# Optimization experiments

Measured on AMD Instinct MI355X. Metric: run time of the kernel, lower is better.

Reference implementation:

```python
import jax, jax.numpy as jnp
import numpy as np

B, M, D = 8, 1024, 1024
H = 16
HD = D // H  # 64
F = 4096

def layer_norm(x, gamma, beta, eps=1e-5):
    mu = jnp.mean(x, axis=-1, keepdims=True)
    var = jnp.var(x, axis=-1, keepdims=True)
    return (x - mu) * jax.lax.rsqrt(var + eps) * gamma + beta

def setup_inputs() -> dict:
    key = jax.random.key(0)
    ks = jax.random.split(key, 16)
    s = 0.02
    return {
        "h": jax.random.normal(ks[0], (B, M, D), jnp.float32),
        "h_all": jax.random.normal(ks[1], (B, M, D), jnp.float32),
        "Wq": jax.random.normal(ks[2], (D, D), jnp.float32) * s,
        "Wk": jax.random.normal(ks[3], (D, D), jnp.float32) * s,
        "Wv": jax.random.normal(ks[4], (D, D), jnp.float32) * s,
        "Wo": jax.random.normal(ks[5], (D, D), jnp.float32) * s,
        "W1": jax.random.normal(ks[6], (D, F), jnp.float32) * s,
        "b1": jnp.zeros((F,), jnp.float32),
        "W2": jax.random.normal(ks[7], (F, D), jnp.float32) * s,
        "b2": jnp.zeros((D,), jnp.float32),
        "g1": jnp.ones((D,), jnp.float32),
        "be1": jnp.zeros((D,), jnp.float32),
        "g2": jnp.ones((D,), jnp.float32),
        "be2": jnp.zeros((D,), jnp.float32),
    }

def reference(h, h_all, Wq, Wk, Wv, Wo, W1, b1, W2, b2, g1, be1, g2, be2):
    Bx, Mx, Dx = h.shape
    # projections (no bias, per nn.Linear(bias=False))
    q = (h @ Wq).reshape(Bx, Mx, H, HD)        # [B,M,H,hd]
    k = (h_all @ Wk).reshape(Bx, -1, H, HD)    # [B,N,H,hd]
    v = (h_all @ Wv).reshape(Bx, -1, H, HD)
    # attention: scale by sqrt(head_dim) as in SeqAttention(hidden_size=head_dim)
    scores = jnp.einsum('bqhd,bkhd->bhqk', q, k) / jnp.sqrt(jnp.float32(HD))
    attn = jax.nn.softmax(scores, axis=-1)
    ctx = jnp.einsum('bhqk,bkhd->bqhd', attn, v).reshape(Bx, Mx, Dx)
    attn_out = ctx @ Wo
    # post-norm residual 1
    h1 = layer_norm(h + attn_out, g1, be1)
    # FFN
    ff = jax.nn.relu(h1 @ W1 + b1) @ W2 + b2
    # post-norm residual 2
    out = layer_norm(h1 + ff, g2, be2)
    return out
```

## Files before the change

### kernel.cpp

```cpp
#include <hip/hip_runtime.h>
#include <hip/hip_bf16.h>

#define ROWS 8192
#define DD   1024
#define HH   16
#define HD   64
#define FF   4096

typedef __attribute__((ext_vector_type(4))) float f32x4;
typedef __attribute__((ext_vector_type(8))) __bf16 bf16x8;

static __device__ __forceinline__ unsigned short f2bf(float f) {
  unsigned u = __float_as_uint(f);
  u += 0x7fffu + ((u >> 16) & 1u);
  return (unsigned short)(u >> 16);
}

static __device__ __forceinline__ float bf2f(unsigned short u) {
  return __uint_as_float(((unsigned)u) << 16);
}

static __device__ __forceinline__ unsigned cvtpk_bf16(float lo, float hi) {
  unsigned r;
  asm("v_cvt_pk_bf16_f32 %0, %1, %2" : "=v"(r) : "v"(lo), "v"(hi));
  return r;
}

static __device__ __forceinline__ f32x4 mfma16(bf16x8 a, bf16x8 b, f32x4 c) {
  return __builtin_amdgcn_mfma_f32_16x16x32_bf16(a, b, c, 0, 0, 0);
}

#define GLOAD16(gp, lp) __builtin_amdgcn_global_load_lds( \
    (__attribute__((address_space(1))) void*)(gp), \
    (__attribute__((address_space(3))) void*)(lp), 16, 0, 0)

__global__ __launch_bounds__(256) void prep_k(
    const float* __restrict__ h, const float* __restrict__ hall,
    const float* __restrict__ Wq, const float* __restrict__ Wk,
    const float* __restrict__ Wv, const float* __restrict__ Wo,
    const float* __restrict__ W1, const float* __restrict__ W2,
    unsigned short* __restrict__ hb, unsigned short* __restrict__ hab,
    unsigned short* __restrict__ wqt, unsigned short* __restrict__ wkvt,
    unsigned short* __restrict__ wot, unsigned short* __restrict__ w1t,
    unsigned short* __restrict__ w2t) {
  __shared__ unsigned short tile[64][66];
  const int bid = blockIdx.x;
  const int tid = threadIdx.x;

  if (bid < 16384) {
    const float* src = (bid < 8192) ? h : hall;
    unsigned short* dst = (bid < 8192) ? hb : hab;
    int i = (bid & 8191) * 256 + tid;
    float4 v = ((const float4*)src)[i];
    ushort4 o;
    o.x = f2bf(v.x); o.y = f2bf(v.y); o.z = f2bf(v.z); o.w = f2bf(v.w);
    ((ushort4*)dst)[i] = o;
    return;
  }

  int r = bid - 16384;
  const float* src; unsigned short* dst; int R, C, bx, by;
  if (r < 1024) {
    int which = r >> 8, idx = r & 255;
    R = C = 1024; bx = idx & 15; by = idx >> 4;
    if (which == 0) { src = Wq; dst = wqt; }
    else if (which == 1) { src = Wk; dst = wkvt; }
    else if (which == 2) { src = Wv; dst = wkvt + (size_t)DD * DD; }
    else { src = Wo; dst = wot; }
  } else if (r < 2048) {
    int idx = r - 1024;
    R = 1024; C = 4096; bx = idx & 63; by = idx >> 6;
    src = W1; dst = w1t;
  } else {
    int idx = r - 2048;
    R = 4096; C = 1024; bx = idx & 15; by = idx >> 4;
    src = W2; dst = w2t;
  }
  const int col = tid & 63, q4 = tid >> 6;
  #pragma unroll
  for (int i = 0; i < 16; ++i) {
    int rr = q4 + i * 4;
    tile[rr][col] = f2bf(src[(size_t)(by * 64 + rr) * C + bx * 64 + col]);
  }
  __syncthreads();
  #pragma unroll
  for (int i = 0; i < 16; ++i) {
    int c = q4 + i * 4;
    dst[(size_t)(bx * 64 + c) * R + by * 64 + col] = tile[col][c];
  }
}

template <int BM, int MODE, int KS = 1>
static __device__ __forceinline__ void gemm_body(
    char* ldsA, char* ldsB,
    const unsigned short* __restrict__ A, const unsigned short* __restrict__ BT,
    const float* __restrict__ bias, void* __restrict__ Cout, void* __restrict__ Cout2,
    int Ni, int Ki, int nbx, int wg, int nwg) {
  constexpr int MR = BM / 32;

  const int tid  = threadIdx.x;
  const int lane = tid & 63;
  const int wid  = tid >> 6;
  const int wm   = wid >> 2;
  const int wn   = wid & 3;
  const int lr   = lane & 15;
  const int kq   = lane >> 4;
  const int axor = (lr & 7) << 4;

  const int cpx = nwg >> 3;
  const int swz = (wg & 7) * cpx + (wg >> 3);
  const int perk = nwg / KS;
  const int kh   = swz / perk;
  const int swzr = swz % perk;
  const int bx = swzr % nbx, by = swzr / nbx;
  const int brow = by * BM, bcol = bx * 256;
  const int Kc   = Ki / KS;
  const int kbase = kh * Kc;

  f32x4 acc[MR][4] = {};
  const int NT = Kc >> 6;

  if constexpr (BM == 256) {
    const size_t loff = (size_t)(lane >> 3) * Ki + ((lane & 7) ^ (lane >> 3)) * 8;
    const unsigned short* Ab = A + (size_t)brow * Ki + kbase;
    const unsigned short* Bb = BT + (size_t)bcol * Ki + kbase;

    auto stage2 = [&](int qc, int u, int db) {
      const int ra = ((wid & 4) << 5) + qc * 32 + (wid & 3) * 8;
      GLOAD16(Ab + (size_t)ra * Ki + u * 64 + loff, ldsA + db * 32768 + ra * 128);
      const int rb = qc * 64 + wid * 8;
      GLOAD16(Bb + (size_t)rb * Ki + u * 64 + loff, ldsB + db * 32768 + rb * 128);
    };

    #pragma unroll
    for (int qc = 0; qc < 4; ++qc) stage2(qc, 0, 0);
    {
      const int u1 = (1 < NT) ? 1 : NT - 1;
      stage2(0, u1, 1); stage2(1, u1, 1); stage2(2, u1, 1);
    }
    asm volatile("s_waitcnt vmcnt(6)" ::: "memory");
    __builtin_amdgcn_s_barrier();
    __builtin_amdgcn_sched_barrier(0);

    #pragma unroll 1
    for (int t = 0; t < NT; ++t) {
      const int d = t & 1;
      const char* ab = ldsA + d * 32768;
      const char* bb = ldsB + d * 32768;
      bf16x8 bfv[4][2];
      #pragma unroll
      for (int q = 0; q < 4; ++q) {
        bf16x8 af[2][2];
        #pragma unroll
        for (int mm = 0; mm < 2; ++mm)
          #pragma unroll
          for (int ks = 0; ks < 2; ++ks)
            af[mm][ks] = *(const bf16x8*)(ab +
                (wm * 128 + (q * 2 + mm) * 16 + lr) * 128 +
                ((ks * 64 + kq * 16) ^ axor));
        if (q == 0) {
          #pragma unroll
          for (int n = 0; n < 4; ++n)
            #pragma unroll
            for (int ks = 0; ks < 2; ++ks)
              bfv[n][ks] = *(const bf16x8*)(bb +
                  (wn * 64 + n * 16 + lr) * 128 +
                  ((ks * 64 + kq * 16) ^ axor));
        }
        if (q == 0) {
          stage2(3, (t + 1 < NT) ? t + 1 : NT - 1, (t + 1) & 1);
        } else {
          stage2(q - 1, (t + 2 < NT) ? t + 2 : NT - 1, d);
        }
        __builtin_amdgcn_s_setprio(1);
        #pragma unroll
        for (int mm = 0; mm < 2; ++mm)
          #pragma unroll
          for (int n = 0; n < 4; ++n) {
            acc[q * 2 + mm][n] = mfma16(af[mm][0], bfv[n][0], acc[q * 2 + mm][n]);
            acc[q * 2 + mm][n] = mfma16(af[mm][1], bfv[n][1], acc[q * 2 + mm][n]);
          }
        __builtin_amdgcn_s_setprio(0);
        __builtin_amdgcn_sched_barrier(0);
        if (q == 3) asm volatile("s_waitcnt vmcnt(6)" ::: "memory");
        __builtin_amdgcn_s_barrier();
        __builtin_amdgcn_sched_barrier(0);
      }
    }
    asm volatile("s_waitcnt vmcnt(0)" ::: "memory");
  } else {
    const int srow = wid * 8 + (lane >> 3);
    const int scol = ((lane & 7) * 8) ^ ((srow & 7) << 3);
    size_t offA[BM / 64], offB[4];
    #pragma unroll
    for (int L = 0; L < BM / 64; ++L)
      offA[L] = (size_t)(brow + L * 64 + srow) * Ki + kbase + scol;
    #pragma unroll
    for (int L = 0; L < 4; ++L)
      offB[L] = (size_t)(bcol + L * 64 + srow) * Ki + kbase + scol;

    auto stage = [&](int t, int d) {
      #pragma unroll
      for (int L = 0; L < BM / 64; ++L)
        GLOAD16(A + offA[L] + t * 64, ldsA + d * (BM * 128) + L * 8192 + wid * 1024);
      #pragma unroll
      for (int L = 0; L < 4; ++L)
        GLOAD16(BT + offB[L] + t * 64, ldsB + d * 32768 + L * 8192 + wid * 1024);
    };

    stage(0, 0);
    stage(1, 1);

    #pragma unroll 1
    for (int t = 0; t < NT; ++t) {
      const int d = t & 1;
      asm volatile("s_waitcnt vmcnt(6)" ::: "memory");
      __builtin_amdgcn_s_barrier();
      __builtin_amdgcn_sched_barrier(0);

      const char* as = ldsA + d * (BM * 128);
      const char* bs = ldsB + d * 32768;
      #pragma unroll
      for (int kk = 0; kk < 2; ++kk) {
        bf16x8 af[MR], bfv[4];
        #pragma unroll
        for (int m = 0; m < MR; ++m)
          af[m] = *(const bf16x8*)(as +
              (wm * (BM / 2) + m * 16 + lr) * 128 + ((kk * 64 + kq * 16) ^ axor));
        #pragma unroll
        for (int n = 0; n < 4; ++n)
          bfv[n] = *(const bf16x8*)(bs +
              (wn * 64 + n * 16 + lr) * 128 + ((kk * 64 + kq * 16) ^ axor));
        #pragma unroll
        for (int m = 0; m < MR; ++m)
          #pragma unroll
          for (int n = 0; n < 4; ++n)
            acc[m][n] = mfma16(af[m], bfv[n], acc[m][n]);
      }

      asm volatile("s_waitcnt lgkmcnt(0)" ::: "memory");
      __builtin_amdgcn_s_barrier();
      __builtin_amdgcn_sched_barrier(0);
      const int ts = (t + 2 < NT) ? t + 2 : NT - 1;
      stage(ts, d);
    }
  }

  #pragma unroll
  for (int m = 0; m < MR; ++m) {
    #pragma unroll
    for (int n = 0; n < 4; ++n) {
      const int r0 = brow + wm * (BM / 2) + m * 16 + kq * 4;
      const int c  = bcol + wn * 64 + n * 16 + lr;
      if constexpr (MODE == 4) {
        if (c < 1024) {
          #pragma unroll
          for (int e = 0; e < 4; ++e)
            ((unsigned short*)Cout)[(size_t)(r0 + e) * 1024 + c] = f2bf(acc[m][n][e]);
        } else {
          const int cc = c - 1024;
          const int bq = r0 >> 10;
          const int tok = r0 & 1023;
          ushort4 pk;
          pk.x = f2bf(acc[m][n][0]); pk.y = f2bf(acc[m][n][1]);
          pk.z = f2bf(acc[m][n][2]); pk.w = f2bf(acc[m][n][3]);
          *(ushort4*)((unsigned short*)Cout2 + ((size_t)bq * 1024 + cc) * 1024 + tok) = pk;
        }
      } else if constexpr (MODE == 5) {
        unsigned short* o = (kh == 0) ? (unsigned short*)Cout : (unsigned short*)Cout2;
        #pragma unroll
        for (int e = 0; e < 4; ++e)
          o[(size_t)(r0 + e) * Ni + c] = f2bf(acc[m][n][e]);
      } else {
        const float bv = (MODE == 2 || MODE == 3) ? bias[c] : 0.0f;
        #pragma unroll
        for (int e = 0; e < 4; ++e) {
          float v = acc[m][n][e] + bv;
          if (MODE == 2) v = fmaxf(v, 0.0f);
          if (MODE == 0 || MODE == 2)
            ((unsigned short*)Cout)[(size_t)(r0 + e) * Ni + c] = f2bf(v);
          else
            ((float*)Cout)[(size_t)(r0 + e) * Ni + c] = v;
        }
      }
    }
  }
}

template <int BM, int MODE, int KS = 1>
__global__ __launch_bounds__(512, 2) void gemm256(
    const unsigned short* __restrict__ A, const unsigned short* __restrict__ BT,
    const float* __restrict__ bias, void* __restrict__ Cout, void* __restrict__ Cout2,
    int Ni, int Ki, int nbx) {
  constexpr int ABYTES = 2 * BM * 64 * 2;
  __shared__ char lds[ABYTES + 65536];
  gemm_body<BM, MODE, KS>(lds, lds + ABYTES, A, BT, bias, Cout, Cout2,
                          Ni, Ki, nbx, (int)blockIdx.x, (int)gridDim.x);
}

__global__ __launch_bounds__(512, 2) void qkv_k(
    const unsigned short* __restrict__ hb, const unsigned short* __restrict__ hab,
    const unsigned short* __restrict__ wqt, const unsigned short* __restrict__ wkvt,
    unsigned short* __restrict__ qb, unsigned short* __restrict__ kb,
    unsigned short* __restrict__ vTb) {
  __shared__ char lds[131072];
  if (blockIdx.x < 256)
    gemm_body<256, 4, 1>(lds, lds + 65536, hab, wkvt, nullptr, kb, vTb,
                         2048, 1024, 8, (int)blockIdx.x, 256);
  else
    gemm_body<128, 0, 1>(lds, lds + 32768, hb, wqt, nullptr, qb, nullptr,
                         1024, 1024, 4, (int)blockIdx.x - 256, 256);
}

__global__ __launch_bounds__(512, 6) void attn_k(
    const unsigned short* __restrict__ q, const unsigned short* __restrict__ k,
    const unsigned short* __restrict__ vT, unsigned short* __restrict__ ctx) {
  __shared__ unsigned short Ks[2][64 * 64];
  __shared__ unsigned short Vt[2][64 * 64];
  __shared__ unsigned short Ps[8][16 * 64];
  const int tid = threadIdx.x;
  const int lane = tid & 63;
  const int wid = tid >> 6;
  const int bh = blockIdx.x;
  const int b = bh >> 4, h = bh & 15;
  const int qrow0 = blockIdx.y * 128 + wid * 16;
  const size_t tokbase = (size_t)b * 1024;
  const int lr = lane & 15, kq = lane >> 4;

  const int srow = tid >> 3;
  const int scol = ((tid & 7) * 8) ^ ((srow & 7) << 3);
  const unsigned short* kg = k + (tokbase + srow) * 1024 + h * 64 + scol;
  const unsigned short* vg = vT + ((size_t)(b * 16 + h) * 64 + srow) * 1024 + scol;
  const int ldst = tid * 16;

  auto stage = [&](int kt, int d) {
    GLOAD16(kg + (size_t)kt * 64 * 1024, (char*)Ks[d] + ldst);
    GLOAD16(vg + kt * 64, (char*)Vt[d] + ldst);
  };

  bf16x8 aq[2];
  {
    const unsigned short* qp = q + (tokbase + qrow0 + lr) * DD + h * 64 + kq * 8;
    aq[0] = *(const bf16x8*)qp;
    aq[1] = *(const bf16x8*)(qp + 32);
  }

  float l_acc = 0.f;
  f32x4 acc[4] = {};
  const float C = 0.125f * 1.4426950408889634f;
  const unsigned swp = (unsigned)((lr & 7) << 4);
  const unsigned pbase = (unsigned)(lr * 128);

  stage(0, 0);
  stage(1, 1);

  #pragma unroll 2
  for (int kt = 0; kt < 16; ++kt) {
    const int d = kt & 1;
    asm volatile("s_waitcnt vmcnt(2)" ::: "memory");
    __builtin_amdgcn_s_barrier();
    __builtin_amdgcn_sched_barrier(0);

    f32x4 sv[4] = {};
    __builtin_amdgcn_s_setprio(1);
    #pragma unroll
    for (int jb = 0; jb < 4; ++jb)
      #pragma unroll
      for (int ks = 0; ks < 2; ++ks) {
        int row = jb * 16 + lr;
        bf16x8 ak = *(const bf16x8*)((const char*)Ks[d] +
            row * 128 + ((ks * 64 + kq * 16) ^ ((row & 7) << 4)));
        sv[jb] = mfma16(ak, aq[ks], sv[jb]);
      }
    __builtin_amdgcn_s_setprio(0);

    #pragma unroll
    for (int jb = 0; jb < 4; ++jb) {
      float p0 = exp2f(sv[jb][0] * C);
      float p1 = exp2f(sv[jb][1] * C);
      float p2 = exp2f(sv[jb][2] * C);
      float p3 = exp2f(sv[jb][3] * C);
      l_acc += (p0 + p1) + (p2 + p3);
      uint2 w;
      w.x = cvtpk_bf16(p0, p1);
      w.y = cvtpk_bf16(p2, p3);
      unsigned off = pbase + (((unsigned)(jb * 32 + kq * 8)) ^ swp);
      *(uint2*)((char*)Ps[wid] + off) = w;
    }

    __builtin_amdgcn_s_setprio(1);
    #pragma unroll
    for (int ks = 0; ks < 2; ++ks) {
      bf16x8 ap = *(const bf16x8*)((const char*)Ps[wid] +
          lr * 128 + ((ks * 64 + kq * 16) ^ ((lr & 7) << 4)));
      #pragma unroll
      for (int db = 0; db < 4; ++db) {
        int dd = db * 16 + lr;
        bf16x8 bv = *(const bf16x8*)((const char*)Vt[d] +
            dd * 128 + ((ks * 64 + kq * 16) ^ ((dd & 7) << 4)));
        acc[db] = mfma16(bv, ap, acc[db]);
      }
    }
    __builtin_amdgcn_s_setprio(0);

    asm volatile("s_waitcnt lgkmcnt(0)" ::: "memory");
    __builtin_amdgcn_s_barrier();
    __builtin_amdgcn_sched_barrier(0);
    const int ts = (kt + 2 < 16) ? kt + 2 : 15;
    stage(ts, d);
  }

  float l = l_acc + __shfl_xor(l_acc, 16);
  l += __shfl_xor(l, 32);
  const float inv = 1.0f / l;
  unsigned short* cp = ctx + (tokbase + qrow0 + lr) * DD + h * 64 + kq * 4;
  #pragma unroll
  for (int db = 0; db < 4; ++db) {
    ushort4 o;
    o.x = f2bf(acc[db][0] * inv);
    o.y = f2bf(acc[db][1] * inv);
    o.z = f2bf(acc[db][2] * inv);
    o.w = f2bf(acc[db][3] * inv);
    *(ushort4*)(cp + db * 16) = o;
  }
}

__global__ __launch_bounds__(256) void ln_add_bb_k(
    const unsigned short* __restrict__ a, const unsigned short* __restrict__ b,
    const float* __restrict__ gamma, const float* __restrict__ beta,
    unsigned short* __restrict__ outb) {
  int row = blockIdx.x;
  int tid = threadIdx.x;
  size_t base = (size_t)row * 1024 + tid * 4;
  ushort4 va = *(const ushort4*)(a + base);
  ushort4 vb = *(const ushort4*)(b + base);
  float x[4] = {bf2f(va.x) + bf2f(vb.x), bf2f(va.y) + bf2f(vb.y),
                bf2f(va.z) + bf2f(vb.z), bf2f(va.w) + bf2f(vb.w)};
  float s = x[0] + x[1] + x[2] + x[3];
  float sq = x[0] * x[0] + x[1] * x[1] + x[2] * x[2] + x[3] * x[3];
  #pragma unroll
  for (int mk = 1; mk < 64; mk <<= 1) {
    s += __shfl_xor(s, mk);
    sq += __shfl_xor(sq, mk);
  }
  __shared__ float red[8];
  int wid = tid >> 6, lane = tid & 63;
  if (lane == 0) { red[wid] = s; red[4 + wid] = sq; }
  __syncthreads();
  s = red[0] + red[1] + red[2] + red[3];
  sq = red[4] + red[5] + red[6] + red[7];
  float mu = s * (1.0f / 1024.0f);
  float var = sq * (1.0f / 1024.0f) - mu * mu;
  float rs = rsqrtf(var + 1e-5f);
  float4 g = *(const float4*)(gamma + tid * 4);
  float4 be = *(const float4*)(beta + tid * 4);
  ushort4 ob;
  ob.x = f2bf((x[0] - mu) * rs * g.x + be.x);
  ob.y = f2bf((x[1] - mu) * rs * g.y + be.y);
  ob.z = f2bf((x[2] - mu) * rs * g.z + be.z);
  ob.w = f2bf((x[3] - mu) * rs * g.w + be.w);
  *(ushort4*)(outb + base) = ob;
}

__global__ __launch_bounds__(256) void ln3_k(
    const unsigned short* __restrict__ a, const unsigned short* __restrict__ p0,
    const unsigned short* __restrict__ p1, const float* __restrict__ b2,
    const float* __restrict__ gamma, const float* __restrict__ beta,
    float* __restrict__ outf) {
  int row = blockIdx.x;
  int tid = threadIdx.x;
  size_t base = (size_t)row * 1024 + tid * 4;
  ushort4 va = *(const ushort4*)(a + base);
  ushort4 v0 = *(const ushort4*)(p0 + base);
  ushort4 v1 = *(const ushort4*)(p1 + base);
  float4 bb = *(const float4*)(b2 + tid * 4);
  float x[4] = {bf2f(va.x) + bf2f(v0.x) + bf2f(v1.x) + bb.x,
                bf2f(va.y) + bf2f(v0.y) + bf2f(v1.y) + bb.y,
                bf2f(va.z) + bf2f(v0.z) + bf2f(v1.z) + bb.z,
                bf2f(va.w) + bf2f(v0.w) + bf2f(v1.w) + bb.w};
  float s = x[0] + x[1] + x[2] + x[3];
  float sq = x[0] * x[0] + x[1] * x[1] + x[2] * x[2] + x[3] * x[3];
  #pragma unroll
  for (int mk = 1; mk < 64; mk <<= 1) {
    s += __shfl_xor(s, mk);
    sq += __shfl_xor(sq, mk);
  }
  __shared__ float red[8];
  int wid = tid >> 6, lane = tid & 63;
  if (lane == 0) { red[wid] = s; red[4 + wid] = sq; }
  __syncthreads();
  s = red[0] + red[1] + red[2] + red[3];
  sq = red[4] + red[5] + red[6] + red[7];
  float mu = s * (1.0f / 1024.0f);
  float var = sq * (1.0f / 1024.0f) - mu * mu;
  float rs = rsqrtf(var + 1e-5f);
  float4 g = *(const float4*)(gamma + tid * 4);
  float4 be = *(const float4*)(beta + tid * 4);
  float4 o;
  o.x = (x[0] - mu) * rs * g.x + be.x;
  o.y = (x[1] - mu) * rs * g.y + be.y;
  o.z = (x[2] - mu) * rs * g.z + be.z;
  o.w = (x[3] - mu) * rs * g.w + be.w;
  *(float4*)(outf + base) = o;
}

extern "C" void kernel_launch(void* const* d_in, const int* in_sizes, int n_in,
                              void* d_out, int out_size, void* d_ws, size_t ws_size,
                              hipStream_t stream) {
  const float* h    = (const float*)d_in[0];
  const float* hall = (const float*)d_in[1];
  const float* Wq   = (const float*)d_in[2];
  const float* Wk   = (const float*)d_in[3];
  const float* Wv   = (const float*)d_in[4];
  const float* Wo   = (const float*)d_in[5];
  const float* W1   = (const float*)d_in[6];
  const float* b1   = (const float*)d_in[7];
  const float* W2   = (const float*)d_in[8];
  const float* b2   = (const float*)d_in[9];
  const float* g1   = (const float*)d_in[10];
  const float* be1  = (const float*)d_in[11];
  const float* g2   = (const float*)d_in[12];
  const float* be2  = (const float*)d_in[13];

  char* ws = (char*)d_ws;
  size_t off = 0;
  auto alloc = [&](size_t n) { size_t o = off; off += (n + 255) & ~(size_t)255; return o; };
  const size_t hb_o   = alloc((size_t)ROWS * DD * 2);
  const size_t hab_o  = alloc((size_t)ROWS * DD * 2);
  const size_t wqt_o  = alloc((size_t)DD * DD * 2);
  const size_t wkvt_o = alloc((size_t)DD * DD * 4);
  const size_t wot_o  = alloc((size_t)DD * DD * 2);
  const size_t w1t_o  = alloc((size_t)DD * FF * 2);
  const size_t w2t_o  = alloc((size_t)FF * DD * 2);
  const size_t qb_o   = alloc((size_t)ROWS * DD * 2);
  const size_t kb_o   = alloc((size_t)ROWS * DD * 2);
  const size_t vt_o   = alloc((size_t)ROWS * DD * 2);
  const size_t cx_o   = alloc((size_t)ROWS * DD * 2);
  const size_t h1b_o  = alloc((size_t)ROWS * DD * 2);
  const size_t fp1_o  = alloc((size_t)ROWS * DD * 2);

  unsigned short* hb   = (unsigned short*)(ws + hb_o);
  unsigned short* hab  = (unsigned short*)(ws + hab_o);
  unsigned short* wqt  = (unsigned short*)(ws + wqt_o);
  unsigned short* wkvt = (unsigned short*)(ws + wkvt_o);
  unsigned short* wot  = (unsigned short*)(ws + wot_o);
  unsigned short* w1t  = (unsigned short*)(ws + w1t_o);
  unsigned short* w2t  = (unsigned short*)(ws + w2t_o);
  unsigned short* qb   = (unsigned short*)(ws + qb_o);
  unsigned short* kb   = (unsigned short*)(ws + kb_o);
  unsigned short* vTb  = (unsigned short*)(ws + vt_o);
  unsigned short* cxb  = (unsigned short*)(ws + cx_o);
  unsigned short* h1b  = (unsigned short*)(ws + h1b_o);
  unsigned short* fp1b = (unsigned short*)(ws + fp1_o);
  unsigned short* attn_ob = (unsigned short*)(ws + hab_o);
  unsigned short* fp0b    = (unsigned short*)(ws + hb_o);
  unsigned short* ff1     = (unsigned short*)(ws + qb_o);
  float*          outf    = (float*)d_out;

  prep_k<<<dim3(16384 + 3072), 256, 0, stream>>>(
      h, hall, Wq, Wk, Wv, Wo, W1, W2, hb, hab, wqt, wkvt, wot, w1t, w2t);

  qkv_k<<<dim3(512), 512, 0, stream>>>(hb, hab, wqt, wkvt, qb, kb, vTb);

  attn_k<<<dim3(128, 8), 512, 0, stream>>>(qb, kb, vTb, cxb);

  gemm256<128, 0><<<dim3(256), 512, 0, stream>>>(cxb, wot, nullptr, attn_ob, nullptr, DD, DD, 4);
  ln_add_bb_k<<<ROWS, 256, 0, stream>>>(hb, attn_ob, g1, be1, h1b);

  gemm256<256, 2>   <<<dim3(512), 512, 0, stream>>>(h1b, w1t, b1, ff1, nullptr, FF, DD, 16);
  gemm256<256, 5, 2><<<dim3(256), 512, 0, stream>>>(ff1, w2t, nullptr, fp0b, fp1b, DD, FF, 4);

  ln3_k<<<ROWS, 256, 0, stream>>>(h1b, fp0b, fp1b, b2, g2, be2, outf);
}
```

Before: 334.7 us.

## Process two query tiles per wave in attention to reuse staged K/V

Each wave in the attention kernel now handles 32 query rows (two 16-row groups) instead of 16, so each block covers 256 queries and the grid halves along the query dimension. The K and V tiles staged into LDS are reused across twice as many queries, which halves global K/V traffic and the barrier count per query. In exchange it uses more registers (occupancy hint lowered from 6 to 4 blocks per CU), a larger P buffer in LDS, and half as many blocks, which may reduce latency hiding.

```diff
diff --git a/kernel.cpp b/kernel.cpp
--- a/kernel.cpp
+++ b/kernel.cpp
@@ -312,18 +312,18 @@
                          1024, 1024, 4, (int)blockIdx.x - 256, 256);
 }
 
-__global__ __launch_bounds__(512, 6) void attn_k(
+__global__ __launch_bounds__(512, 4) void attn_k(
     const unsigned short* __restrict__ q, const unsigned short* __restrict__ k,
     const unsigned short* __restrict__ vT, unsigned short* __restrict__ ctx) {
   __shared__ unsigned short Ks[2][64 * 64];
   __shared__ unsigned short Vt[2][64 * 64];
-  __shared__ unsigned short Ps[8][16 * 64];
+  __shared__ unsigned short Ps[8][32 * 64];
   const int tid = threadIdx.x;
   const int lane = tid & 63;
   const int wid = tid >> 6;
   const int bh = blockIdx.x;
   const int b = bh >> 4, h = bh & 15;
-  const int qrow0 = blockIdx.y * 128 + wid * 16;
+  const int qrow0 = blockIdx.y * 256 + wid * 32;
   const size_t tokbase = (size_t)b * 1024;
   const int lr = lane & 15, kq = lane >> 4;
 
@@ -338,18 +338,19 @@
     GLOAD16(vg + kt * 64, (char*)Vt[d] + ldst);
   };
 
-  bf16x8 aq[2];
-  {
-    const unsigned short* qp = q + (tokbase + qrow0 + lr) * DD + h * 64 + kq * 8;
-    aq[0] = *(const bf16x8*)qp;
-    aq[1] = *(const bf16x8*)(qp + 32);
-  }
-
-  float l_acc = 0.f;
-  f32x4 acc[4] = {};
+  bf16x8 aq[2][2];
+  #pragma unroll
+  for (int g = 0; g < 2; ++g) {
+    const unsigned short* qp =
+        q + (tokbase + qrow0 + g * 16 + lr) * DD + h * 64 + kq * 8;
+    aq[g][0] = *(const bf16x8*)qp;
+    aq[g][1] = *(const bf16x8*)(qp + 32);
+  }
+
+  float l_acc[2] = {0.f, 0.f};
+  f32x4 acc[2][4] = {};
   const float C = 0.125f * 1.4426950408889634f;
   const unsigned swp = (unsigned)((lr & 7) << 4);
-  const unsigned pbase = (unsigned)(lr * 128);
 
   stage(0, 0);
   stage(1, 1);
@@ -361,47 +362,51 @@
     __builtin_amdgcn_s_barrier();
     __builtin_amdgcn_sched_barrier(0);
 
-    f32x4 sv[4] = {};
-    __builtin_amdgcn_s_setprio(1);
     #pragma unroll
-    for (int jb = 0; jb < 4; ++jb)
+    for (int g = 0; g < 2; ++g) {
+      f32x4 sv[4] = {};
+      __builtin_amdgcn_s_setprio(1);
+      #pragma unroll
+      for (int jb = 0; jb < 4; ++jb)
+        #pragma unroll
+        for (int ks = 0; ks < 2; ++ks) {
+          int row = jb * 16 + lr;
+          bf16x8 ak = *(const bf16x8*)((const char*)Ks[d] +
+              row * 128 + ((ks * 64 + kq * 16) ^ ((row & 7) << 4)));
+          sv[jb] = mfma16(ak, aq[g][ks], sv[jb]);
+        }
+      __builtin_amdgcn_s_setprio(0);
+
+      const unsigned pbase = (unsigned)((g * 16 + lr) * 128);
+      #pragma unroll
+      for (int jb = 0; jb < 4; ++jb) {
+        float p0 = exp2f(sv[jb][0] * C);
+        float p1 = exp2f(sv[jb][1] * C);
+        float p2 = exp2f(sv[jb][2] * C);
+        float p3 = exp2f(sv[jb][3] * C);
+        l_acc[g] += (p0 + p1) + (p2 + p3);
+        uint2 w;
+        w.x = cvtpk_bf16(p0, p1);
+        w.y = cvtpk_bf16(p2, p3);
+        unsigned off = pbase + (((unsigned)(jb * 32 + kq * 8)) ^ swp);
+        *(uint2*)((char*)Ps[wid] + off) = w;
+      }
+
+      __builtin_amdgcn_s_setprio(1);
       #pragma unroll
       for (int ks = 0; ks < 2; ++ks) {
-        int row = jb * 16 + lr;
-        bf16x8 ak = *(const bf16x8*)((const char*)Ks[d] +
-            row * 128 + ((ks * 64 + kq * 16) ^ ((row & 7) << 4)));
-        sv[jb] = mfma16(ak, aq[ks], sv[jb]);
+        bf16x8 ap = *(const bf16x8*)((const char*)Ps[wid] +
+            (g * 16 + lr) * 128 + ((ks * 64 + kq * 16) ^ ((lr & 7) << 4)));
+        #pragma unroll
+        for (int db = 0; db < 4; ++db) {
+          int dd = db * 16 + lr;
+          bf16x8 bv = *(const bf16x8*)((const char*)Vt[d] +
+              dd * 128 + ((ks * 64 + kq * 16) ^ ((dd & 7) << 4)));
+          acc[g][db] = mfma16(bv, ap, acc[g][db]);
+        }
       }
-    __builtin_amdgcn_s_setprio(0);
-
-    #pragma unroll
-    for (int jb = 0; jb < 4; ++jb) {
-      float p0 = exp2f(sv[jb][0] * C);
-      float p1 = exp2f(sv[jb][1] * C);
-      float p2 = exp2f(sv[jb][2] * C);
-      float p3 = exp2f(sv[jb][3] * C);
-      l_acc += (p0 + p1) + (p2 + p3);
-      uint2 w;
-      w.x = cvtpk_bf16(p0, p1);
-      w.y = cvtpk_bf16(p2, p3);
-      unsigned off = pbase + (((unsigned)(jb * 32 + kq * 8)) ^ swp);
-      *(uint2*)((char*)Ps[wid] + off) = w;
+      __builtin_amdgcn_s_setprio(0);
     }
-
-    __builtin_amdgcn_s_setprio(1);
-    #pragma unroll
-    for (int ks = 0; ks < 2; ++ks) {
-      bf16x8 ap = *(const bf16x8*)((const char*)Ps[wid] +
-          lr * 128 + ((ks * 64 + kq * 16) ^ ((lr & 7) << 4)));
-      #pragma unroll
-      for (int db = 0; db < 4; ++db) {
-        int dd = db * 16 + lr;
-        bf16x8 bv = *(const bf16x8*)((const char*)Vt[d] +
-            dd * 128 + ((ks * 64 + kq * 16) ^ ((dd & 7) << 4)));
-        acc[db] = mfma16(bv, ap, acc[db]);
-      }
-    }
-    __builtin_amdgcn_s_setprio(0);
 
     asm volatile("s_waitcnt lgkmcnt(0)" ::: "memory");
     __builtin_amdgcn_s_barrier();
@@ -410,18 +415,22 @@
     stage(ts, d);
   }
 
-  float l = l_acc + __shfl_xor(l_acc, 16);
-  l += __shfl_xor(l, 32);
-  const float inv = 1.0f / l;
-  unsigned short* cp = ctx + (tokbase + qrow0 + lr) * DD + h * 64 + kq * 4;
-  #pragma unroll
-  for (int db = 0; db < 4; ++db) {
-    ushort4 o;
-    o.x = f2bf(acc[db][0] * inv);
-    o.y = f2bf(acc[db][1] * inv);
-    o.z = f2bf(acc[db][2] * inv);
-    o.w = f2bf(acc[db][3] * inv);
-    *(ushort4*)(cp + db * 16) = o;
+  #pragma unroll
+  for (int g = 0; g < 2; ++g) {
+    float l = l_acc[g] + __shfl_xor(l_acc[g], 16);
+    l += __shfl_xor(l, 32);
+    const float inv = 1.0f / l;
+    unsigned short* cp =
+        ctx + (tokbase + qrow0 + g * 16 + lr) * DD + h * 64 + kq * 4;
+    #pragma unroll
+    for (int db = 0; db < 4; ++db) {
+      ushort4 o;
+      o.x = f2bf(acc[g][db][0] * inv);
+      o.y = f2bf(acc[g][db][1] * inv);
+      o.z = f2bf(acc[g][db][2] * inv);
+      o.w = f2bf(acc[g][db][3] * inv);
+      *(ushort4*)(cp + db * 16) = o;
+    }
   }
 }
 
@@ -562,7 +571,7 @@
 
   qkv_k<<<dim3(512), 512, 0, stream>>>(hb, hab, wqt, wkvt, qb, kb, vTb);
 
-  attn_k<<<dim3(128, 8), 512, 0, stream>>>(qb, kb, vTb, cxb);
+  attn_k<<<dim3(128, 4), 512, 0, stream>>>(qb, kb, vTb, cxb);
 
   gemm256<128, 0><<<dim3(256), 512, 0, stream>>>(cxb, wot, nullptr, attn_ob, nullptr, DD, DD, 4);
   ln_add_bb_k<<<ROWS, 256, 0, stream>>>(hb, attn_ob, g1, be1, h1b);
```

New measurement: 501.1 us. 1.5x slower.
